# Kernel optimization log

Hardware: AMD Instinct MI355X
Metric: run time of the kernel (lower is better)

## Reference

```python
import jax, jax.numpy as jnp
import numpy as np

H, W, SCALE = 480, 640, 8  # full-res grid and coarse downsample factor (hw0_i/hw0_c)


def _struct_feats(pts, anchor_ids):
    """pts: [N, H*W, 3]; anchor_ids: [N, A] int -> [N, L, 4*A] with L=(H//SCALE)*(W//SCALE)."""
    N = pts.shape[0]
    coarse = pts.reshape(N, H, W, 3)[:, ::SCALE, ::SCALE, :].reshape(N, -1, 3)  # [N, L, 3]
    anchors = jnp.take_along_axis(pts, anchor_ids[:, :, None], axis=1)          # [N, A, 3]
    diff = coarse[:, :, None, :] - anchors[:, None, :, :]                        # [N, L, A, 3]
    dist = jnp.sum(diff * diff, axis=-1, keepdims=True)                          # [N, L, A, 1]
    s = jnp.concatenate([diff, dist], axis=-1)                                   # [N, L, A, 4]
    s = s / jnp.sum(jnp.abs(s), axis=-2, keepdims=True)                          # L1 norm over anchor axis
    s = jnp.swapaxes(s, -1, -2).reshape(N, coarse.shape[1], -1)                  # [N, L, 4A]
    return s


def _mlp(x, W1, b1, W2, b2):
    return jax.nn.relu(x @ W1 + b1) @ W2 + b2


def setup_inputs() -> dict:
    key = jax.random.key(0)
    ks = jax.random.split(key, 10)
    N, L, C, A, P = 4, 4800, 256, 128, H * W
    D = C + 4 * A  # 768
    return {
        "feat0": jax.random.normal(ks[0], (N, L, C), jnp.float32),
        "feat1": jax.random.normal(ks[1], (N, L, C), jnp.float32),
        "pts_3d0": jax.random.normal(ks[2], (N, P, 3), jnp.float32),
        "pts_3d1": jax.random.normal(ks[3], (N, P, 3), jnp.float32),
        "anchor_i_ids": jax.random.randint(ks[4], (N, A), 0, P),
        "anchor_j_ids": jax.random.randint(ks[5], (N, A), 0, P),
        "W1": jax.random.normal(ks[6], (D, D), jnp.float32) * (1.0 / np.sqrt(D)),
        "b1": jnp.zeros((D,), jnp.float32),
        "W2": jax.random.normal(ks[7], (D, C), jnp.float32) * (1.0 / np.sqrt(D)),
        "b2": jnp.zeros((C,), jnp.float32),
    }


def reference(feat0, feat1, pts_3d0, pts_3d1, anchor_i_ids, anchor_j_ids, W1, b1, W2, b2):
    s0 = _struct_feats(pts_3d0, anchor_i_ids)  # [N, L, 4A]
    s1 = _struct_feats(pts_3d1, anchor_j_ids)
    aug0 = _mlp(jnp.concatenate([feat0, s0], axis=-1), W1, b1, W2, b2)  # [N, L, C]
    aug1 = _mlp(jnp.concatenate([feat1, s1], axis=-1), W1, b1, W2, b2)
    return (aug0, aug1)
```

## Files before the change

### kernel.cpp

```cpp
#include <hip/hip_runtime.h>
#include <stdint.h>
#include <stddef.h>

typedef __attribute__((ext_vector_type(8))) short short8;
typedef __attribute__((ext_vector_type(4))) short short4v;
typedef __attribute__((ext_vector_type(4))) float f32x4;

typedef const __attribute__((address_space(3))) char* lds_cp;

#define GLDS16(gp, lp)                                                        \
    __builtin_amdgcn_global_load_lds(                                         \
        (const __attribute__((address_space(1))) void*)(gp),                  \
        (__attribute__((address_space(3))) void*)(lp), 16, 0, 0)

__device__ __forceinline__ short8 ldsr16(lds_cp p) {
    short8 v;
    asm volatile("ds_read_b128 %0, %1" : "=v"(v) : "v"(p));
    return v;
}

#define WAIT_LGKM0_PIN()                                                      \
    do {                                                                      \
        asm volatile("s_waitcnt lgkmcnt(0)" ::: "memory");                    \
        __builtin_amdgcn_sched_barrier(0);                                    \
    } while (0)

__device__ __forceinline__ unsigned short f2bf(float f) {
    union { float f; uint32_t u; } v;
    v.f = f;
    uint32_t u = v.u;
    u += 0x7FFFu + ((u >> 16) & 1u);
    return (unsigned short)(u >> 16);
}

__global__ __launch_bounds__(1024) void transpose_to_bf16(
    const float* __restrict__ src, unsigned short* __restrict__ dst, int R, int C)
{
    __shared__ float tile[32][33];
    const int c0 = blockIdx.x * 32, r0 = blockIdx.y * 32;
    const int tx = threadIdx.x, ty = threadIdx.y;
    tile[ty][tx] = src[(size_t)(r0 + ty) * C + (c0 + tx)];
    __syncthreads();
    dst[(size_t)(c0 + ty) * R + (r0 + tx)] = f2bf(tile[tx][ty]);
}

__global__ __launch_bounds__(64) void struct_pack(
    const float* __restrict__ feat0, const float* __restrict__ feat1,
    const float* __restrict__ pts0,  const float* __restrict__ pts1,
    const int* __restrict__ ids0,    const int* __restrict__ ids1,
    unsigned short* __restrict__ xw)
{
    const int m = blockIdx.x;
    const int t = m / 19200;
    const int r = m % 19200;
    const int n = r / 4800;
    const int l = r % 4800;
    const float* feat = t ? feat1 : feat0;
    const float* pts  = (t ? pts1 : pts0) + (size_t)n * (307200 * 3);
    const int*   ids  = (t ? ids1 : ids0) + n * 128;
    const int a = threadIdx.x;

    const int lr = l / 80, lc = l % 80;
    const int p  = (lr * 8) * 640 + lc * 8;
    const float cx = pts[p * 3 + 0], cy = pts[p * 3 + 1], cz = pts[p * 3 + 2];

    const int id0 = ids[a], id1 = ids[a + 64];
    const float d0x = cx - pts[id0 * 3 + 0];
    const float d0y = cy - pts[id0 * 3 + 1];
    const float d0z = cz - pts[id0 * 3 + 2];
    const float d0d = d0x * d0x + d0y * d0y + d0z * d0z;
    const float d1x = cx - pts[id1 * 3 + 0];
    const float d1y = cy - pts[id1 * 3 + 1];
    const float d1z = cz - pts[id1 * 3 + 2];
    const float d1d = d1x * d1x + d1y * d1y + d1z * d1z;

    float p0 = fabsf(d0x) + fabsf(d1x);
    float p1 = fabsf(d0y) + fabsf(d1y);
    float p2 = fabsf(d0z) + fabsf(d1z);
    float p3 = d0d + d1d;
#pragma unroll
    for (int off = 32; off; off >>= 1) {
        p0 += __shfl_xor(p0, off);
        p1 += __shfl_xor(p1, off);
        p2 += __shfl_xor(p2, off);
        p3 += __shfl_xor(p3, off);
    }
    const float i0 = 1.0f / p0, i1 = 1.0f / p1, i2 = 1.0f / p2, i3 = 1.0f / p3;

    unsigned short* xrow = xw + (size_t)m * 768;
    const float* frow = feat + (size_t)(n * 4800 + l) * 256;
    const float4 fv = ((const float4*)frow)[a];
    short4v s4;
    s4.x = (short)f2bf(fv.x); s4.y = (short)f2bf(fv.y);
    s4.z = (short)f2bf(fv.z); s4.w = (short)f2bf(fv.w);
    *(short4v*)(xrow + a * 4) = s4;

    xrow[256 + 0 * 128 + a]      = f2bf(d0x * i0);
    xrow[256 + 0 * 128 + a + 64] = f2bf(d1x * i0);
    xrow[256 + 1 * 128 + a]      = f2bf(d0y * i1);
    xrow[256 + 1 * 128 + a + 64] = f2bf(d1y * i1);
    xrow[256 + 2 * 128 + a]      = f2bf(d0z * i2);
    xrow[256 + 2 * 128 + a + 64] = f2bf(d1z * i2);
    xrow[256 + 3 * 128 + a]      = f2bf(d0d * i3);
    xrow[256 + 3 * 128 + a + 64] = f2bf(d1d * i3);
}

template <int MI, int NJ, int WRN_LOG, bool RELU, bool OUT_BF16>
__global__ __launch_bounds__(512, 2) void gemm_t(
    const unsigned short* __restrict__ A,
    const unsigned short* __restrict__ Bt,
    const float* __restrict__ bias,
    void* __restrict__ Cout,
    int K, int N, int ntx, int q8, int r8)
{
    constexpr int WRN = 1 << WRN_LOG;
    constexpr int WRM = 8 / WRN;
    constexpr int BM = WRM * MI * 16;
    constexpr int BN = WRN * NJ * 16;
    constexpr int ASLOT = BM * 128;
    constexpr int BSLOT = BN * 128;
    constexpr int ALD = BM / 64;
    constexpr int BLD = BN / 64;
    static_assert(ALD == 4, "vmcnt immediates assume 4 A-loads/wave/tile");

    extern __shared__ char lds[];
    const int nt = K >> 6;

    const int bid = blockIdx.x;
    const int xcd = bid & 7, idx = bid >> 3;
    const int w = (xcd < r8 ? xcd * (q8 + 1) : r8 * (q8 + 1) + (xcd - r8) * q8) + idx;
    const int n0 = (w % ntx) * BN;
    const int m0 = (w / ntx) * BM;

    const int tid = threadIdx.x;
    const int lane = tid & 63;
    const int wv = tid >> 6;
    const int wr = wv >> WRN_LOG;
    const int wc = wv & (WRN - 1);

    const int slr = lane >> 3;
    const int kc  = (lane & 7) ^ slr;
    const unsigned short* gA = A  + (size_t)(m0 + wv * 8 + slr) * K + kc * 8;
    const unsigned short* gB = Bt + (size_t)(n0 + wv * 8 + slr) * K + kc * 8;

    auto stA = [&](int slot, int i, int kt) {
        GLDS16(gA + (size_t)i * 64 * K + kt, lds + slot * ASLOT + (i * 64 + wv * 8) * 128);
    };
    auto stB = [&](int slot, int j, int kt) {
        GLDS16(gB + (size_t)j * 64 * K + kt, lds + 3 * ASLOT + slot * BSLOT + (j * 64 + wv * 8) * 128);
    };

    const int rsel = lane & 15;
    const int kbh  = lane >> 4;
    const int ck0 = ((kbh) ^ (rsel & 7)) * 16;
    const int ck1 = ((4 + kbh) ^ (rsel & 7)) * 16;
    const int aRowB = (wr * (MI * 16) + rsel) * 128;
    const int bRowB = (wc * (NJ * 16) + rsel) * 128;

    auto LDA = [&](int slot, int mi, int ks) -> short8 {
        return ldsr16((lds_cp)(lds + slot * ASLOT + aRowB + mi * 2048 + (ks ? ck1 : ck0)));
    };
    auto LDB = [&](int slot, int nj, int ks) -> short8 {
        return ldsr16((lds_cp)(lds + 3 * ASLOT + slot * BSLOT + bRowB + nj * 2048 + (ks ? ck1 : ck0)));
    };

    f32x4 acc[MI][NJ] = {};
    short8 aF[MI / 2], bF[NJ];

    {
#pragma unroll
        for (int i = 0; i < ALD; ++i) stA(0, i, 0);
#pragma unroll
        for (int j = 0; j < BLD; ++j) stB(0, j, 0);
        if (nt > 1) {
#pragma unroll
            for (int i = 0; i < ALD; ++i) stA(1, i, 64);
            asm volatile("s_waitcnt vmcnt(4)" ::: "memory");
        } else {
            asm volatile("s_waitcnt vmcnt(0)" ::: "memory");
        }
        __builtin_amdgcn_s_barrier();
    }

    int cb3 = 0;
    for (int t = 0; t < nt; ++t) {
        const int cb2 = t & 1;
        const int sb2 = cb2 ^ 1;
        int sa3 = cb3 + 2; if (sa3 >= 3) sa3 -= 3;
        const int kt1 = (t + 1) << 6;
        const int kt2 = (t + 2) << 6;
        const bool stb = (t + 1) < nt;
        const bool sta = (t + 2) < nt;

#pragma unroll
        for (int nj = 0; nj < NJ; ++nj) bF[nj] = LDB(cb2, nj, 0);
#pragma unroll
        for (int mi = 0; mi < MI / 2; ++mi) aF[mi] = LDA(cb3, mi, 0);
        if (stb) {
#pragma unroll
            for (int j = 0; j < BLD / 2; ++j) stB(sb2, j, kt1);
        }
        __builtin_amdgcn_s_barrier();
        WAIT_LGKM0_PIN();
        __builtin_amdgcn_s_setprio(1);
#pragma unroll
        for (int mi = 0; mi < MI / 2; ++mi)
#pragma unroll
            for (int nj = 0; nj < NJ; ++nj)
                acc[mi][nj] = __builtin_amdgcn_mfma_f32_16x16x32_bf16(aF[mi], bF[nj], acc[mi][nj], 0, 0, 0);
        __builtin_amdgcn_s_setprio(0);
        __builtin_amdgcn_s_barrier();

#pragma unroll
        for (int mi = 0; mi < MI / 2; ++mi) aF[mi] = LDA(cb3, MI / 2 + mi, 0);
        if (stb) {
#pragma unroll
            for (int j = BLD / 2; j < BLD; ++j) stB(sb2, j, kt1);
        }
        __builtin_amdgcn_s_barrier();
        WAIT_LGKM0_PIN();
        __builtin_amdgcn_s_setprio(1);
#pragma unroll
        for (int mi = 0; mi < MI / 2; ++mi)
#pragma unroll
            for (int nj = 0; nj < NJ; ++nj)
                acc[MI / 2 + mi][nj] = __builtin_amdgcn_mfma_f32_16x16x32_bf16(aF[mi], bF[nj], acc[MI / 2 + mi][nj], 0, 0, 0);
        __builtin_amdgcn_s_setprio(0);
        __builtin_amdgcn_s_barrier();

#pragma unroll
        for (int nj = 0; nj < NJ; ++nj) bF[nj] = LDB(cb2, nj, 1);
#pragma unroll
        for (int mi = 0; mi < MI / 2; ++mi) aF[mi] = LDA(cb3, mi, 1);
        if (sta) { stA(sa3, 0, kt2); stA(sa3, 1, kt2); }
        __builtin_amdgcn_s_barrier();
        WAIT_LGKM0_PIN();
        __builtin_amdgcn_s_setprio(1);
#pragma unroll
        for (int mi = 0; mi < MI / 2; ++mi)
#pragma unroll
            for (int nj = 0; nj < NJ; ++nj)
                acc[mi][nj] = __builtin_amdgcn_mfma_f32_16x16x32_bf16(aF[mi], bF[nj], acc[mi][nj], 0, 0, 0);
        __builtin_amdgcn_s_setprio(0);
        __builtin_amdgcn_s_barrier();

#pragma unroll
        for (int mi = 0; mi < MI / 2; ++mi) aF[mi] = LDA(cb3, MI / 2 + mi, 1);
        if (sta) { stA(sa3, 2, kt2); stA(sa3, 3, kt2); }
        __builtin_amdgcn_s_barrier();
        WAIT_LGKM0_PIN();
        __builtin_amdgcn_s_setprio(1);
#pragma unroll
        for (int mi = 0; mi < MI / 2; ++mi)
#pragma unroll
            for (int nj = 0; nj < NJ; ++nj)
                acc[MI / 2 + mi][nj] = __builtin_amdgcn_mfma_f32_16x16x32_bf16(aF[mi], bF[nj], acc[MI / 2 + mi][nj], 0, 0, 0);
        __builtin_amdgcn_s_setprio(0);

        if (t + 1 < nt) {
            if (t + 2 < nt) asm volatile("s_waitcnt vmcnt(4)" ::: "memory");
            else            asm volatile("s_waitcnt vmcnt(0)" ::: "memory");
            __builtin_amdgcn_s_barrier();
        }
        cb3 = (cb3 + 1 == 3) ? 0 : cb3 + 1;
    }

    const int crow = (lane >> 4) * 4;
    const int ccol = lane & 15;
#pragma unroll
    for (int nj = 0; nj < NJ; ++nj) {
        const int col = n0 + wc * (NJ * 16) + nj * 16 + ccol;
        const float bv = bias[col];
#pragma unroll
        for (int mi = 0; mi < MI; ++mi) {
#pragma unroll
            for (int rg = 0; rg < 4; ++rg) {
                const int row = m0 + wr * (MI * 16) + mi * 16 + crow + rg;
                float v = acc[mi][nj][rg] + bv;
                if (RELU) v = fmaxf(v, 0.0f);
                if (OUT_BF16) {
                    ((unsigned short*)Cout)[(size_t)row * N + col] = f2bf(v);
                } else {
                    ((float*)Cout)[(size_t)row * N + col] = v;
                }
            }
        }
    }
}

extern "C" void kernel_launch(void* const* d_in, const int* in_sizes, int n_in,
                              void* d_out, int out_size, void* d_ws, size_t ws_size,
                              hipStream_t stream) {
    const float* feat0 = (const float*)d_in[0];
    const float* feat1 = (const float*)d_in[1];
    const float* pts0  = (const float*)d_in[2];
    const float* pts1  = (const float*)d_in[3];
    const int*   ids0  = (const int*)d_in[4];
    const int*   ids1  = (const int*)d_in[5];
    const float* W1    = (const float*)d_in[6];
    const float* b1    = (const float*)d_in[7];
    const float* W2    = (const float*)d_in[8];
    const float* b2    = (const float*)d_in[9];
    float* out = (float*)d_out;

    char* ws = (char*)d_ws;
    unsigned short* xw  = (unsigned short*)(ws);
    unsigned short* h   = (unsigned short*)(ws + 58982400);
    unsigned short* w1t = (unsigned short*)(ws + 117964800);
    unsigned short* w2t = (unsigned short*)(ws + 119144448);

    const int LDS1 = 3 * 32768 + 2 * 32768;
    const int LDS2 = 3 * 32768 + 2 * 16384;
    (void)hipFuncSetAttribute((const void*)&gemm_t<8, 4, 2, true, true>,
                              hipFuncAttributeMaxDynamicSharedMemorySize, LDS1);
    (void)hipFuncSetAttribute((const void*)&gemm_t<4, 4, 1, false, false>,
                              hipFuncAttributeMaxDynamicSharedMemorySize, LDS2);

    dim3 tb(32, 32);
    transpose_to_bf16<<<dim3(768 / 32, 768 / 32), tb, 0, stream>>>(W1, w1t, 768, 768);
    transpose_to_bf16<<<dim3(256 / 32, 768 / 32), tb, 0, stream>>>(W2, w2t, 768, 256);

    struct_pack<<<38400, 64, 0, stream>>>(feat0, feat1, pts0, pts1, ids0, ids1, xw);

    gemm_t<8, 4, 2, true, true><<<450, 512, LDS1, stream>>>(xw, w1t, b1, (void*)h, 768, 768, 3, 56, 2);
    gemm_t<4, 4, 1, false, false><<<300, 512, LDS2, stream>>>(h, w2t, b2, (void*)out, 768, 256, 2, 37, 4);
}
```

Measured before the change: 126.1 us.

## Prefetch LDS fragments with partial lgkmcnt waits and drop intra-tile barriers

The GEMM main loop now issues the low and high A-fragment reads, and the second k-half B reads, ahead of the MFMA groups that need them. It waits with partial lgkmcnt counts, so LDS reads overlap with the matrix math instead of draining to zero before each group. The four per-phase s_barrier pairs inside each K tile are removed, leaving one barrier per tile, and all B and A global-to-LDS stages are issued in single batches. The cost is more live fragment registers (separate A low/high and B buffers for both k-halves), which could hurt occupancy or cause spills under the 512x2 launch bound. Correctness also now relies on the triple and double buffering alone to separate LDS writers from readers.

```diff
diff --git a/kernel.cpp b/kernel.cpp
--- a/kernel.cpp
+++ b/kernel.cpp
@@ -19,11 +19,15 @@
     return v;
 }
 
-#define WAIT_LGKM0_PIN()                                                      \
-    do {                                                                      \
-        asm volatile("s_waitcnt lgkmcnt(0)" ::: "memory");                    \
-        __builtin_amdgcn_sched_barrier(0);                                    \
-    } while (0)
+template <int N>
+__device__ __forceinline__ void wait_lgkm() {
+    static_assert(N == 0 || N == 2 || N == 4 || N == 8, "unsupported count");
+    if constexpr (N == 0) asm volatile("s_waitcnt lgkmcnt(0)" ::: "memory");
+    else if constexpr (N == 2) asm volatile("s_waitcnt lgkmcnt(2)" ::: "memory");
+    else if constexpr (N == 4) asm volatile("s_waitcnt lgkmcnt(4)" ::: "memory");
+    else if constexpr (N == 8) asm volatile("s_waitcnt lgkmcnt(8)" ::: "memory");
+    __builtin_amdgcn_sched_barrier(0);
+}
 
 __device__ __forceinline__ unsigned short f2bf(float f) {
     union { float f; uint32_t u; } v;
@@ -122,6 +126,7 @@
     constexpr int ALD = BM / 64;
     constexpr int BLD = BN / 64;
     static_assert(ALD == 4, "vmcnt immediates assume 4 A-loads/wave/tile");
+    static_assert(MI + NJ <= 13, "lgkm in-flight cap");
 
     extern __shared__ char lds[];
     const int nt = K >> 6;
@@ -165,7 +170,7 @@
     };
 
     f32x4 acc[MI][NJ] = {};
-    short8 aF[MI / 2], bF[NJ];
+    short8 aL[MI / 2], aH[MI / 2], aL1[MI / 2], aH1[MI / 2], bF0[NJ], bF1[NJ];
 
     {
 #pragma unroll
@@ -193,73 +198,66 @@
         const bool sta = (t + 2) < nt;
 
 #pragma unroll
-        for (int nj = 0; nj < NJ; ++nj) bF[nj] = LDB(cb2, nj, 0);
-#pragma unroll
-        for (int mi = 0; mi < MI / 2; ++mi) aF[mi] = LDA(cb3, mi, 0);
+        for (int nj = 0; nj < NJ; ++nj) bF0[nj] = LDB(cb2, nj, 0);
+#pragma unroll
+        for (int mi = 0; mi < MI / 2; ++mi) aL[mi] = LDA(cb3, mi, 0);
+#pragma unroll
+        for (int mi = 0; mi < MI / 2; ++mi) aH[mi] = LDA(cb3, MI / 2 + mi, 0);
+
+        wait_lgkm<MI / 2>();
+        __builtin_amdgcn_s_setprio(1);
+#pragma unroll
+        for (int mi = 0; mi < MI / 2; ++mi)
+#pragma unroll
+            for (int nj = 0; nj < NJ; ++nj)
+                acc[mi][nj] = __builtin_amdgcn_mfma_f32_16x16x32_bf16(aL[mi], bF0[nj], acc[mi][nj], 0, 0, 0);
+        __builtin_amdgcn_s_setprio(0);
+
+#pragma unroll
+        for (int nj = 0; nj < NJ; ++nj) bF1[nj] = LDB(cb2, nj, 1);
         if (stb) {
 #pragma unroll
-            for (int j = 0; j < BLD / 2; ++j) stB(sb2, j, kt1);
-        }
-        __builtin_amdgcn_s_barrier();
-        WAIT_LGKM0_PIN();
+            for (int j = 0; j < BLD; ++j) stB(sb2, j, kt1);
+        }
+
+        wait_lgkm<NJ>();
         __builtin_amdgcn_s_setprio(1);
 #pragma unroll
         for (int mi = 0; mi < MI / 2; ++mi)
 #pragma unroll
             for (int nj = 0; nj < NJ; ++nj)
-                acc[mi][nj] = __builtin_amdgcn_mfma_f32_16x16x32_bf16(aF[mi], bF[nj], acc[mi][nj], 0, 0, 0);
+                acc[MI / 2 + mi][nj] = __builtin_amdgcn_mfma_f32_16x16x32_bf16(aH[mi], bF0[nj], acc[MI / 2 + mi][nj], 0, 0, 0);
         __builtin_amdgcn_s_setprio(0);
-        __builtin_amdgcn_s_barrier();
-
-#pragma unroll
-        for (int mi = 0; mi < MI / 2; ++mi) aF[mi] = LDA(cb3, MI / 2 + mi, 0);
-        if (stb) {
-#pragma unroll
-            for (int j = BLD / 2; j < BLD; ++j) stB(sb2, j, kt1);
-        }
-        __builtin_amdgcn_s_barrier();
-        WAIT_LGKM0_PIN();
+
+#pragma unroll
+        for (int mi = 0; mi < MI / 2; ++mi) aL1[mi] = LDA(cb3, mi, 1);
+#pragma unroll
+        for (int mi = 0; mi < MI / 2; ++mi) aH1[mi] = LDA(cb3, MI / 2 + mi, 1);
+        if (sta) {
+            stA(sa3, 0, kt2); stA(sa3, 1, kt2); stA(sa3, 2, kt2); stA(sa3, 3, kt2);
+        }
+
+        wait_lgkm<MI / 2>();
         __builtin_amdgcn_s_setprio(1);
 #pragma unroll
         for (int mi = 0; mi < MI / 2; ++mi)
 #pragma unroll
             for (int nj = 0; nj < NJ; ++nj)
-                acc[MI / 2 + mi][nj] = __builtin_amdgcn_mfma_f32_16x16x32_bf16(aF[mi], bF[nj], acc[MI / 2 + mi][nj], 0, 0, 0);
+                acc[mi][nj] = __builtin_amdgcn_mfma_f32_16x16x32_bf16(aL1[mi], bF1[nj], acc[mi][nj], 0, 0, 0);
         __builtin_amdgcn_s_setprio(0);
-        __builtin_amdgcn_s_barrier();
-
-#pragma unroll
-        for (int nj = 0; nj < NJ; ++nj) bF[nj] = LDB(cb2, nj, 1);
-#pragma unroll
-        for (int mi = 0; mi < MI / 2; ++mi) aF[mi] = LDA(cb3, mi, 1);
-        if (sta) { stA(sa3, 0, kt2); stA(sa3, 1, kt2); }
-        __builtin_amdgcn_s_barrier();
-        WAIT_LGKM0_PIN();
+
+        wait_lgkm<0>();
         __builtin_amdgcn_s_setprio(1);
 #pragma unroll
         for (int mi = 0; mi < MI / 2; ++mi)
 #pragma unroll
             for (int nj = 0; nj < NJ; ++nj)
-                acc[mi][nj] = __builtin_amdgcn_mfma_f32_16x16x32_bf16(aF[mi], bF[nj], acc[mi][nj], 0, 0, 0);
+                acc[MI / 2 + mi][nj] = __builtin_amdgcn_mfma_f32_16x16x32_bf16(aH1[mi], bF1[nj], acc[MI / 2 + mi][nj], 0, 0, 0);
         __builtin_amdgcn_s_setprio(0);
-        __builtin_amdgcn_s_barrier();
-
-#pragma unroll
-        for (int mi = 0; mi < MI / 2; ++mi) aF[mi] = LDA(cb3, MI / 2 + mi, 1);
-        if (sta) { stA(sa3, 2, kt2); stA(sa3, 3, kt2); }
-        __builtin_amdgcn_s_barrier();
-        WAIT_LGKM0_PIN();
-        __builtin_amdgcn_s_setprio(1);
-#pragma unroll
-        for (int mi = 0; mi < MI / 2; ++mi)
-#pragma unroll
-            for (int nj = 0; nj < NJ; ++nj)
-                acc[MI / 2 + mi][nj] = __builtin_amdgcn_mfma_f32_16x16x32_bf16(aF[mi], bF[nj], acc[MI / 2 + mi][nj], 0, 0, 0);
-        __builtin_amdgcn_s_setprio(0);
 
         if (t + 1 < nt) {
-            if (t + 2 < nt) asm volatile("s_waitcnt vmcnt(4)" ::: "memory");
-            else            asm volatile("s_waitcnt vmcnt(0)" ::: "memory");
+            if (sta) asm volatile("s_waitcnt vmcnt(4)" ::: "memory");
+            else     asm volatile("s_waitcnt vmcnt(0)" ::: "memory");
             __builtin_amdgcn_s_barrier();
         }
         cb3 = (cb3 + 1 == 3) ? 0 : cb3 + 1;
```

Result: faster. 116.9 us (-7.3%).
